# Kernel tuning notes

Measured on AMD Instinct MI355X. Metric: run time of the kernel, lower is better.

Reference implementation:

```python
import jax, jax.numpy as jnp
import numpy as np

B = 8192          # number of jagged segments
SUF = 256         # suffix length appended per segment


def setup_inputs() -> dict:
    key = jax.random.key(0)
    k1, k2 = jax.random.split(key)
    rng = np.random.RandomState(0)
    lengths = rng.randint(1024, 3072, size=B).astype(np.int64)  # mean ~2048
    prefix_sum = np.cumsum(lengths)                              # inclusive prefix sum
    n_vals = int(prefix_sum[-1])
    values = jax.random.normal(k1, (n_vals,), dtype=jnp.float32)
    suffix_mat = jax.random.normal(k2, (B, SUF), dtype=jnp.float32)
    return {
        "values": values,
        "prefix_sum": jnp.asarray(prefix_sum, dtype=jnp.int64),
        "suffix_mat": suffix_mat,
    }


def reference(values, prefix_sum, suffix_mat):
    # Jagged append: out = concat_i( values[seg_i] ++ suffix_mat[i] )
    b, suf = suffix_mat.shape
    n_vals = values.shape[0]
    n_out = n_vals + b * suf
    # inclusive prefix sum of output segment lengths (each old len + suf)
    new_prefix = prefix_sum + (jnp.arange(1, b + 1, dtype=prefix_sum.dtype)) * suf
    j = jnp.arange(n_out, dtype=prefix_sum.dtype)
    # segment id for each output position
    seg = jnp.searchsorted(new_prefix, j, side="right")
    prev_old = jnp.where(seg > 0, prefix_sum[jnp.maximum(seg - 1, 0)], 0)  # old start offset
    new_start = prev_old + seg * suf                                        # new start offset
    local = j - new_start                                                   # pos within out segment
    seg_len = prefix_sum[seg] - prev_old                                    # old segment length
    in_vals = local < seg_len
    val_idx = jnp.clip(prev_old + local, 0, n_vals - 1)
    suf_idx = jnp.clip(local - seg_len, 0, suf - 1)
    return jnp.where(in_vals, values[val_idx], suffix_mat[seg, suf_idx])
```

## Files before the change

kernel.cpp:

```cpp
#include <hip/hip_runtime.h>


#define SUF 256

__global__ void jagged_append_kernel(const float* __restrict__ values,
                                     const int* __restrict__ prefix_sum,
                                     const float* __restrict__ suffix,
                                     float* __restrict__ out,
                                     int B) {
    const int seg = blockIdx.x;
    if (seg >= B) return;

    const long long prev_old = (seg > 0) ? (long long)prefix_sum[seg - 1] : 0ll;
    const long long end_old  = (long long)prefix_sum[seg];
    const long long seg_len  = end_old - prev_old;
    const long long new_start = prev_old + (long long)seg * SUF;

    for (long long i = threadIdx.x; i < seg_len; i += blockDim.x) {
        out[new_start + i] = values[prev_old + i];
    }

    const float* sfx = suffix + (long long)seg * SUF;
    const long long suf_base = new_start + seg_len;
    for (int i = threadIdx.x; i < SUF; i += blockDim.x) {
        out[suf_base + i] = sfx[i];
    }
}

extern "C" void kernel_launch(void* const* d_in, const int* in_sizes, int n_in,
                              void* d_out, int out_size, void* d_ws, size_t ws_size,
                              hipStream_t stream) {
    const float* values     = (const float*)d_in[0];
    const int*   prefix_sum = (const int*)d_in[1];
    const float* suffix     = (const float*)d_in[2];
    float* out = (float*)d_out;

    const int B = in_sizes[1];

    jagged_append_kernel<<<B, 256, 0, stream>>>(values, prefix_sum, suffix, out, B);
}
```

Measured before the change: 29.78 us.

## Split output into fixed-size chunks with binary search and vectorized copies

Replaces the one-block-per-segment launch with blocks that each own a fixed 8192-element span of the output. Each block binary-searches the prefix sums to find its starting segment, then walks the segments that overlap its span. Value copies use an alignment-adjusted float4 path, with scalar head and tail handling, because source and destination share the same phase offset. This balances work across blocks regardless of segment length and widens memory transactions, at the cost of a per-block binary search and more branching.

```diff
diff --git a/kernel.cpp b/kernel.cpp
--- a/kernel.cpp
+++ b/kernel.cpp
@@ -2,28 +2,68 @@
 
 
 #define SUF 256
+#define NTHR 256
+#define CHUNK 8192
 
-__global__ void jagged_append_kernel(const float* __restrict__ values,
-                                     const int* __restrict__ prefix_sum,
-                                     const float* __restrict__ suffix,
-                                     float* __restrict__ out,
-                                     int B) {
-    const int seg = blockIdx.x;
-    if (seg >= B) return;
+typedef float floatx4 __attribute__((ext_vector_type(4)));
 
-    const long long prev_old = (seg > 0) ? (long long)prefix_sum[seg - 1] : 0ll;
-    const long long end_old  = (long long)prefix_sum[seg];
-    const long long seg_len  = end_old - prev_old;
-    const long long new_start = prev_old + (long long)seg * SUF;
+__device__ __forceinline__ void copy_same_phase(float* __restrict__ dst,
+                                                const float* __restrict__ src,
+                                                int n, int tid) {
+    int head = (4 - (((unsigned)(size_t)dst >> 2) & 3)) & 3;
+    if (head > n) head = n;
+    if (tid < head) dst[tid] = src[tid];
+    const int nvec = (n - head) >> 2;
+    const floatx4* __restrict__ vs = (const floatx4*)(src + head);
+    floatx4* __restrict__ vd = (floatx4*)(dst + head);
+    for (int v = tid; v < nvec; v += NTHR) vd[v] = vs[v];
+    for (int i = head + (nvec << 2) + tid; i < n; i += NTHR) dst[i] = src[i];
+}
 
-    for (long long i = threadIdx.x; i < seg_len; i += blockDim.x) {
-        out[new_start + i] = values[prev_old + i];
+__global__ __launch_bounds__(NTHR) void
+jagged_append_flat(const float* __restrict__ values,
+                   const int* __restrict__ prefix_sum,
+                   const float* __restrict__ suffix,
+                   float* __restrict__ out,
+                   int B, int n_out) {
+    const int tid = threadIdx.x;
+    const int span_s = blockIdx.x * CHUNK;
+    if (span_s >= n_out) return;
+    const int span_e = min(span_s + CHUNK, n_out);
+
+    int lo = 0, hi = B - 1;
+    while (lo < hi) {
+        int mid = (lo + hi) >> 1;
+        int np = prefix_sum[mid] + (mid + 1) * SUF;
+        if (np > span_s) hi = mid; else lo = mid + 1;
     }
+    int seg = lo;
+    int ps_prev = (seg > 0) ? prefix_sum[seg - 1] : 0;
 
-    const float* sfx = suffix + (long long)seg * SUF;
-    const long long suf_base = new_start + seg_len;
-    for (int i = threadIdx.x; i < SUF; i += blockDim.x) {
-        out[suf_base + i] = sfx[i];
+    int s = span_s;
+    while (s < span_e && seg < B) {
+        const int ps_cur = prefix_sum[seg];
+        const int new_start = ps_prev + seg * SUF;
+        const int seg_len = ps_cur - ps_prev;
+        const int vals_end = new_start + seg_len;
+        const int seg_end = vals_end + SUF;
+
+        int a = s > new_start ? s : new_start;
+        int b = span_e < vals_end ? span_e : vals_end;
+        if (a < b) copy_same_phase(out + a, values + (a - seg * SUF), b - a, tid);
+
+        int c = s > vals_end ? s : vals_end;
+        int d = span_e < seg_end ? span_e : seg_end;
+        if (c < d) {
+            const float* __restrict__ sf = suffix + seg * SUF + (c - vals_end);
+            float* __restrict__ od = out + c;
+            const int n = d - c;
+            for (int i = tid; i < n; i += NTHR) od[i] = sf[i];
+        }
+
+        s = seg_end;
+        ++seg;
+        ps_prev = ps_cur;
     }
 }
 
@@ -36,6 +76,8 @@
     float* out = (float*)d_out;
 
     const int B = in_sizes[1];
+    const int nblocks = (out_size + CHUNK - 1) / CHUNK;
 
-    jagged_append_kernel<<<B, 256, 0, stream>>>(values, prefix_sum, suffix, out, B);
+    jagged_append_flat<<<nblocks, NTHR, 0, stream>>>(values, prefix_sum, suffix,
+                                                     out, B, out_size);
 }
```

After: 34.90 us. 17.2% more time.
